# Kernel tuning notes

Measured on AMD Instinct MI355X. Metric: run time of the kernel, lower is better.

## Reference

```python
import jax, jax.numpy as jnp
import numpy as np

B, T, F, H = 128, 512, 256, 512


def setup_inputs() -> dict:
    key = jax.random.key(0)
    k1, k2, k3, k4 = jax.random.split(key, 4)
    scale_k = 1.0 / np.sqrt(F)
    scale_r = 1.0 / np.sqrt(H)
    return {
        "x": jax.random.normal(k1, (B, T, F), dtype=jnp.float32),
        "kernel": jax.random.normal(k2, (F, 4 * H), dtype=jnp.float32) * scale_k,
        "recurrent_kernel": jax.random.normal(k3, (H, 4 * H), dtype=jnp.float32) * scale_r,
        "bias": jax.random.normal(k4, (4 * H,), dtype=jnp.float32) * 0.01,
    }


def _lstm(x, kernel, recurrent_kernel, bias):
    # x: [B, T, F] -> scan over time. Keras gate order: i, f, g(cell), o.
    h0 = jnp.zeros((x.shape[0], H), dtype=x.dtype)
    c0 = jnp.zeros((x.shape[0], H), dtype=x.dtype)
    # Precompute input projections for all timesteps in one big GEMM: [B,T,4H]
    xz = jnp.einsum('btf,fg->btg', x, kernel) + bias

    def step(carry, xz_t):
        h, c = carry
        z = xz_t + h @ recurrent_kernel  # [B, 4H]
        i, f, g, o = jnp.split(z, 4, axis=-1)
        i = jax.nn.sigmoid(i)
        f = jax.nn.sigmoid(f)
        g = jnp.tanh(g)
        o = jax.nn.sigmoid(o)
        c_new = f * c + i * g
        h_new = o * jnp.tanh(c_new)
        return (h_new, c_new), h_new

    (h_last, c_last), hs = jax.lax.scan(step, (h0, c0), jnp.swapaxes(xz, 0, 1))
    output = jnp.swapaxes(hs, 0, 1)  # [B, T, H]
    return output, h_last, c_last


def reference(x, kernel, recurrent_kernel, bias):
    # Inference-mode forward (dropout inactive), matching Keras LSTM eval behavior.
    output, h, c = _lstm(x, kernel, recurrent_kernel, bias)
    return (output, h, c)
```

## Files before the change

### kernel.cpp

```cpp
#include <hip/hip_runtime.h>
#include <stdint.h>


#define Bb 128
#define Tt 512
#define Ff 256
#define Hh 512
#define G4 2048
#define SENT 0xFFFFFFFFu

typedef __attribute__((ext_vector_type(8))) short short8;
typedef __attribute__((ext_vector_type(4))) float floatx4;
typedef __attribute__((ext_vector_type(4))) unsigned int uint4v;

__device__ __forceinline__ unsigned short f2bf(float f) {
    unsigned u = __float_as_uint(f);
    return (unsigned short)((u + 0x7FFFu + ((u >> 16) & 1u)) >> 16);
}
__device__ __forceinline__ float bf2f(unsigned short h) {
    return __uint_as_float(((unsigned)h) << 16);
}
__device__ __forceinline__ float sigm(float x) { return 1.f / (1.f + __expf(-x)); }
__device__ __forceinline__ float tanh_f(float x) {
    float e = __expf(-2.f * fabsf(x));
    return copysignf((1.f - e) / (1.f + e), x);
}

__global__ __launch_bounds__(256, 2) void lstm_xz(
    const float* __restrict__ x, const float* __restrict__ w,
    const float* __restrict__ bias, _Float16* __restrict__ xzh)
{
    __shared__ unsigned short Ahi[128 * 40];
    __shared__ unsigned short Alo[128 * 40];
    __shared__ unsigned short Wt [128 * 40];

    const int tid = threadIdx.x;
    int idx = blockIdx.x;
    int xcd = idx & 7;
    int chunk = idx >> 3;
    int msup = chunk >> 7;
    int s = chunk & 127;
    int nt = s >> 3;
    int mi0 = s & 7;
    int mt = xcd * 64 + msup * 8 + mi0;
    const int m0 = mt << 7;
    const int n0 = nt << 7;

    const int lane = tid & 63;
    const int wv = tid >> 6;
    const int wm = wv >> 1, wn = wv & 1;
    const int cB = lane & 15, kgrp = lane >> 4;

    floatx4 acc[4][4];
#pragma unroll
    for (int i = 0; i < 4; ++i)
#pragma unroll
        for (int j = 0; j < 4; ++j) acc[i][j] = (floatx4){0.f, 0.f, 0.f, 0.f};

    float bv[4];
#pragma unroll
    for (int ni = 0; ni < 4; ++ni) bv[ni] = bias[n0 + wn * 64 + ni * 16 + cB];

    for (int it = 0; it < 8; ++it) {
        const int k0 = it * 32;
#pragma unroll
        for (int sw = 0; sw < 4; ++sw) {
            int e = sw * 256 + tid;
            int row = e >> 3, kq = e & 7;
            float4 v = *((const float4*)(x + (size_t)(m0 + row) * Ff + k0) + kq);
            unsigned short h0 = f2bf(v.x), h1 = f2bf(v.y), h2 = f2bf(v.z), h3 = f2bf(v.w);
            unsigned short l0 = f2bf(v.x - bf2f(h0)), l1 = f2bf(v.y - bf2f(h1));
            unsigned short l2 = f2bf(v.z - bf2f(h2)), l3 = f2bf(v.w - bf2f(h3));
            uint2 ph, pl;
            ph.x = (unsigned)h0 | ((unsigned)h1 << 16); ph.y = (unsigned)h2 | ((unsigned)h3 << 16);
            pl.x = (unsigned)l0 | ((unsigned)l1 << 16); pl.y = (unsigned)l2 | ((unsigned)l3 << 16);
            *(uint2*)(&Ahi[row * 40 + kq * 4]) = ph;
            *(uint2*)(&Alo[row * 40 + kq * 4]) = pl;
        }
#pragma unroll
        for (int sw = 0; sw < 4; ++sw) {
            int e = sw * 256 + tid;
            int kr = e >> 5, nq = e & 31;
            float4 v = *((const float4*)(w + (size_t)(k0 + kr) * G4 + n0) + nq);
            int nb = nq * 4;
            Wt[(nb + 0) * 40 + kr] = f2bf(v.x);
            Wt[(nb + 1) * 40 + kr] = f2bf(v.y);
            Wt[(nb + 2) * 40 + kr] = f2bf(v.z);
            Wt[(nb + 3) * 40 + kr] = f2bf(v.w);
        }
        __syncthreads();

        short8 bfr[4];
#pragma unroll
        for (int ni = 0; ni < 4; ++ni)
            bfr[ni] = *(const short8*)(&Wt[(wn * 64 + ni * 16 + cB) * 40 + kgrp * 8]);
#pragma unroll
        for (int mi = 0; mi < 4; ++mi) {
            short8 ah = *(const short8*)(&Ahi[(wm * 64 + mi * 16 + cB) * 40 + kgrp * 8]);
            short8 al = *(const short8*)(&Alo[(wm * 64 + mi * 16 + cB) * 40 + kgrp * 8]);
#pragma unroll
            for (int ni = 0; ni < 4; ++ni) {
                acc[mi][ni] = __builtin_amdgcn_mfma_f32_16x16x32_bf16(ah, bfr[ni], acc[mi][ni], 0, 0, 0);
                acc[mi][ni] = __builtin_amdgcn_mfma_f32_16x16x32_bf16(al, bfr[ni], acc[mi][ni], 0, 0, 0);
            }
        }
        __syncthreads();
    }
#pragma unroll
    for (int mi = 0; mi < 4; ++mi)
#pragma unroll
        for (int ni = 0; ni < 4; ++ni) {
            int rowb = m0 + wm * 64 + mi * 16 + kgrp * 4;
            int col = n0 + wn * 64 + ni * 16 + cB;
#pragma unroll
            for (int rr = 0; rr < 4; ++rr)
                xzh[(size_t)(rowb + rr) * G4 + col] = (_Float16)(acc[mi][ni][rr] + bv[ni]);
        }
}

__global__ __launch_bounds__(256, 1) void lstm_rec(
    const _Float16* __restrict__ xzh, const float* __restrict__ rk,
    unsigned* __restrict__ hbuf_u, float* __restrict__ out)
{
    __shared__ unsigned short Rlds[128 * 512];

    const int tid = threadIdx.x;
    const int idx = blockIdx.x;
    const int rg = idx & 7;
    const int cb = idx >> 3;
    const int b0 = rg * 16;
    const int hc0 = cb * 32;

    const int lane = tid & 63;
    const int wv = tid >> 6;
    const int cB = lane & 15, kgrp = lane >> 4;
    const int hcw = hc0 + wv * 8;
    const int c7 = cB & 7;
    const int col = hcw + c7;
    const bool hi = (cB & 8) != 0;

    for (int e = tid; e < 64 * 512; e += 256) {
        int p = e & 63, k = e >> 6;
        int n0 = 2 * p;
        int loc = n0 & 31, w = n0 >> 5;
        int gate = ((loc >> 4) << 1) | ((loc >> 3) & 1);
        int gcol = gate * Hh + hc0 + w * 8 + (loc & 7);
        float2 v = *(const float2*)(rk + (size_t)k * G4 + gcol);
        Rlds[n0 * 512 + (k ^ ((n0 & 7) << 3))] = f2bf(v.x);
        Rlds[(n0 + 1) * 512 + (k ^ (((n0 + 1) & 7) << 3))] = f2bf(v.y);
    }

    const unsigned* xz_u = (const unsigned*)xzh;
    const unsigned* pr[4];
#pragma unroll
    for (int r = 0; r < 4; ++r)
        pr[r] = xz_u + ((size_t)(b0 + kgrp * 4 + r) * Tt * G4 + (col & ~1)) / 2;

    float xzr[16];
#pragma unroll
    for (int g = 0; g < 4; ++g)
#pragma unroll
        for (int r = 0; r < 4; ++r) {
            unsigned v = pr[r][g * 256];
            xzr[g * 4 + r] = (float)__builtin_bit_cast(_Float16,
                (unsigned short)((col & 1) ? (v >> 16) : (v & 0xffffu)));
        }
#pragma unroll
    for (int r = 0; r < 4; ++r) pr[r] += G4 / 2;

    __syncthreads();

    short8 bf0[16], bf1[16];
    {
        const int nb = wv * 32;
        const int swz = c7 << 3;
#pragma unroll
        for (int kk = 0; kk < 16; ++kk) {
            int kb = (kk * 32 + kgrp * 8) ^ swz;
            bf0[kk] = *(const short8*)&Rlds[(nb + cB) * 512 + kb];
            bf1[kk] = *(const short8*)&Rlds[(nb + 16 + cB) * 512 + kb];
        }
    }
    __syncthreads();

    float creg[4] = {0.f, 0.f, 0.f, 0.f};
    unsigned* const gbase = hbuf_u + (size_t)rg * 4 * 4096;

    for (int t = 0; t < Tt; ++t) {
        const bool last = (t == Tt - 1);

        unsigned pf[16];
        if (!last) {
#pragma unroll
            for (int g = 0; g < 4; ++g)
#pragma unroll
                for (int r = 0; r < 4; ++r)
                    pf[g * 4 + r] = pr[r][g * 256];
        }

        floatx4 acc0 = (floatx4){0.f, 0.f, 0.f, 0.f};
        floatx4 acc1 = (floatx4){0.f, 0.f, 0.f, 0.f};

        if (t > 0) {
            unsigned short* const hs = (t & 1) ? (Rlds + 16 * 512) : Rlds;
            unsigned* const hcu = (unsigned*)hs;

            {
                const unsigned* sb = gbase + ((t - 1) & 3) * 4096;
                const unsigned* q0 = sb + (wv + 0) * 256 + 4 * lane;
                const unsigned* q1 = sb + (wv + 4) * 256 + 4 * lane;
                const unsigned* q2 = sb + (wv + 8) * 256 + 4 * lane;
                const unsigned* q3 = sb + (wv + 12) * 256 + 4 * lane;
                uint4v v0, v1, v2, v3;
                asm volatile("global_load_dwordx4 %0, %1, off sc0 sc1" : "=v"(v0) : "v"(q0) : "memory");
                asm volatile("global_load_dwordx4 %0, %1, off sc0 sc1" : "=v"(v1) : "v"(q1) : "memory");
                asm volatile("global_load_dwordx4 %0, %1, off sc0 sc1" : "=v"(v2) : "v"(q2) : "memory");
                asm volatile("global_load_dwordx4 %0, %1, off sc0 sc1" : "=v"(v3) : "v"(q3) : "memory");
                asm volatile("s_waitcnt vmcnt(0)" ::: "memory");
                while (__any((v0[0] == SENT) | (v0[1] == SENT) | (v0[2] == SENT) | (v0[3] == SENT))) {
                    asm volatile("global_load_dwordx4 %0, %1, off sc0 sc1" : "=v"(v0) : "v"(q0) : "memory");
                    asm volatile("s_waitcnt vmcnt(0)" ::: "memory");
                }
                *(uint4v*)(hcu + (wv + 0) * 256 + 4 * (lane ^ ((wv + 0) & 7))) = v0;
                while (__any((v1[0] == SENT) | (v1[1] == SENT) | (v1[2] == SENT) | (v1[3] == SENT))) {
                    asm volatile("global_load_dwordx4 %0, %1, off sc0 sc1" : "=v"(v1) : "v"(q1) : "memory");
                    asm volatile("s_waitcnt vmcnt(0)" ::: "memory");
                }
                *(uint4v*)(hcu + (wv + 4) * 256 + 4 * (lane ^ ((wv + 4) & 7))) = v1;
                while (__any((v2[0] == SENT) | (v2[1] == SENT) | (v2[2] == SENT) | (v2[3] == SENT))) {
                    asm volatile("global_load_dwordx4 %0, %1, off sc0 sc1" : "=v"(v2) : "v"(q2) : "memory");
                    asm volatile("s_waitcnt vmcnt(0)" ::: "memory");
                }
                *(uint4v*)(hcu + (wv + 8) * 256 + 4 * (lane ^ ((wv + 8) & 7))) = v2;
                while (__any((v3[0] == SENT) | (v3[1] == SENT) | (v3[2] == SENT) | (v3[3] == SENT))) {
                    asm volatile("global_load_dwordx4 %0, %1, off sc0 sc1" : "=v"(v3) : "v"(q3) : "memory");
                    asm volatile("s_waitcnt vmcnt(0)" ::: "memory");
                }
                *(uint4v*)(hcu + (wv + 12) * 256 + 4 * (lane ^ ((wv + 12) & 7))) = v3;
            }

            if (t >= 2) {
                unsigned* rs = gbase + ((t - 2) & 3) * 4096
                             + (tid >> 4) * 256 + (hc0 >> 1) + (tid & 15);
                __hip_atomic_store(rs, SENT, __ATOMIC_RELAXED, __HIP_MEMORY_SCOPE_AGENT);
            }

            __syncthreads();

            floatx4 e0 = (floatx4){0.f, 0.f, 0.f, 0.f};
            floatx4 e1 = (floatx4){0.f, 0.f, 0.f, 0.f};
            const int swz = c7 << 3;
#pragma unroll
            for (int kk = 0; kk < 16; kk += 2) {
                int kb0 = (kk * 32 + kgrp * 8) ^ swz;
                int kb1 = ((kk + 1) * 32 + kgrp * 8) ^ swz;
                short8 a0 = *(const short8*)&hs[cB * 512 + kb0];
                short8 a1 = *(const short8*)&hs[cB * 512 + kb1];
                acc0 = __builtin_amdgcn_mfma_f32_16x16x32_bf16(a0, bf0[kk], acc0, 0, 0, 0);
                acc1 = __builtin_amdgcn_mfma_f32_16x16x32_bf16(a0, bf1[kk], acc1, 0, 0, 0);
                e0 = __builtin_amdgcn_mfma_f32_16x16x32_bf16(a1, bf0[kk + 1], e0, 0, 0, 0);
                e1 = __builtin_amdgcn_mfma_f32_16x16x32_bf16(a1, bf1[kk + 1], e1, 0, 0, 0);
            }
            acc0 = acc0 + e0;
            acc1 = acc1 + e1;
        }

        float hv[4];
#pragma unroll
        for (int r = 0; r < 4; ++r) {
            float a0 = acc0[r], a1 = acc1[r];
            float a0x = __shfl_xor(a0, 8);
            float a1x = __shfl_xor(a1, 8);
            float zi = (hi ? a0x : a0) + xzr[0 * 4 + r];
            float zf = (hi ? a0 : a0x) + xzr[1 * 4 + r];
            float zg = (hi ? a1x : a1) + xzr[2 * 4 + r];
            float zo = (hi ? a1 : a1x) + xzr[3 * 4 + r];
            creg[r] = sigm(zf) * creg[r] + sigm(zi) * tanh_f(zg);
            hv[r] = sigm(zo) * tanh_f(creg[r]);
        }

        float hn[4];
#pragma unroll
        for (int r = 0; r < 4; ++r) hn[r] = __shfl_xor(hv[r], 1);
        const bool ew = (!hi && !(cB & 1));

        if (!last) {
            unsigned* wbase = gbase + (t & 3) * 4096;
#pragma unroll
            for (int r = 0; r < 4; ++r) {
                if (ew) {
                    unsigned hp = (unsigned)f2bf(hv[r]) | ((unsigned)f2bf(hn[r]) << 16);
                    __hip_atomic_store(wbase + (kgrp * 4 + r) * 256 + (col >> 1), hp,
                                       __ATOMIC_RELAXED, __HIP_MEMORY_SCOPE_AGENT);
                }
            }
        }

#pragma unroll
        for (int r = 0; r < 4; ++r) {
            if (ew) {
                size_t b = (size_t)(b0 + kgrp * 4 + r);
                *(float2*)(out + (b * Tt + (size_t)t) * Hh + col) = make_float2(hv[r], hn[r]);
            }
        }

        if (last) {
            float* hl = out + (size_t)Bb * Tt * Hh;
            float* cl = hl + (size_t)Bb * Hh;
#pragma unroll
            for (int r = 0; r < 4; ++r) {
                float cn = __shfl_xor(creg[r], 1);
                if (ew) {
                    size_t b = (size_t)(b0 + kgrp * 4 + r);
                    *(float2*)(hl + b * Hh + col) = make_float2(hv[r], hn[r]);
                    *(float2*)(cl + b * Hh + col) = make_float2(creg[r], cn);
                }
            }
            break;
        }

#pragma unroll
        for (int i = 0; i < 16; ++i)
            xzr[i] = (float)__builtin_bit_cast(_Float16,
                (unsigned short)((col & 1) ? (pf[i] >> 16) : (pf[i] & 0xffffu)));
#pragma unroll
        for (int r = 0; r < 4; ++r) pr[r] += G4 / 2;
    }
}

extern "C" void kernel_launch(void* const* d_in, const int* in_sizes, int n_in,
                              void* d_out, int out_size, void* d_ws, size_t ws_size,
                              hipStream_t stream) {
    (void)in_sizes; (void)n_in; (void)out_size; (void)ws_size;
    const float* x    = (const float*)d_in[0];
    const float* w    = (const float*)d_in[1];
    const float* rk   = (const float*)d_in[2];
    const float* bias = (const float*)d_in[3];
    float* out = (float*)d_out;

    char* ws = (char*)d_ws;
    const size_t XZ_BYTES   = (size_t)Bb * Tt * G4 * sizeof(_Float16);
    const size_t HBUF_BYTES = (size_t)8 * 4 * 16 * 256 * 4;

    _Float16* xzh = (_Float16*)ws;
    unsigned* hbuf = (unsigned*)(ws + XZ_BYTES);

    hipMemsetAsync(ws + XZ_BYTES, 0xFF, HBUF_BYTES, stream);

    lstm_xz<<<dim3(8192), dim3(256), 0, stream>>>(x, w, bias, xzh);
    lstm_rec<<<dim3(128), dim3(256), 0, stream>>>(xzh, rk, hbuf, out);
}
```

Baseline: 2.236 ms.

## Fuse input projection GEMM into recurrent kernel, computing x·W per timestep

Removes the separate xz GEMM kernel and its fp16 intermediate buffer. Each recurrent block now keeps its slice of the input kernel in registers, stages x[t+1] as hi/lo bf16 in LDS (double-buffered), and runs the extra MFMAs each step alongside the hidden-state exchange. This eliminates the large xz write and read and one launch. The cost is extra MFMA work and x loads on the serial critical path of every timestep, using only 128 blocks.

```diff
diff --git a/kernel.cpp b/kernel.cpp
--- a/kernel.cpp
+++ b/kernel.cpp
@@ -8,6 +8,7 @@
 #define Hh 512
 #define G4 2048
 #define SENT 0xFFFFFFFFu
+#define XB 16384
 
 typedef __attribute__((ext_vector_type(8))) short short8;
 typedef __attribute__((ext_vector_type(4))) float floatx4;
@@ -26,100 +27,33 @@
     return copysignf((1.f - e) / (1.f + e), x);
 }
 
-__global__ __launch_bounds__(256, 2) void lstm_xz(
-    const float* __restrict__ x, const float* __restrict__ w,
-    const float* __restrict__ bias, _Float16* __restrict__ xzh)
-{
-    __shared__ unsigned short Ahi[128 * 40];
-    __shared__ unsigned short Alo[128 * 40];
-    __shared__ unsigned short Wt [128 * 40];
-
-    const int tid = threadIdx.x;
-    int idx = blockIdx.x;
-    int xcd = idx & 7;
-    int chunk = idx >> 3;
-    int msup = chunk >> 7;
-    int s = chunk & 127;
-    int nt = s >> 3;
-    int mi0 = s & 7;
-    int mt = xcd * 64 + msup * 8 + mi0;
-    const int m0 = mt << 7;
-    const int n0 = nt << 7;
-
-    const int lane = tid & 63;
-    const int wv = tid >> 6;
-    const int wm = wv >> 1, wn = wv & 1;
-    const int cB = lane & 15, kgrp = lane >> 4;
-
-    floatx4 acc[4][4];
-#pragma unroll
-    for (int i = 0; i < 4; ++i)
-#pragma unroll
-        for (int j = 0; j < 4; ++j) acc[i][j] = (floatx4){0.f, 0.f, 0.f, 0.f};
-
-    float bv[4];
-#pragma unroll
-    for (int ni = 0; ni < 4; ++ni) bv[ni] = bias[n0 + wn * 64 + ni * 16 + cB];
-
-    for (int it = 0; it < 8; ++it) {
-        const int k0 = it * 32;
-#pragma unroll
-        for (int sw = 0; sw < 4; ++sw) {
-            int e = sw * 256 + tid;
-            int row = e >> 3, kq = e & 7;
-            float4 v = *((const float4*)(x + (size_t)(m0 + row) * Ff + k0) + kq);
-            unsigned short h0 = f2bf(v.x), h1 = f2bf(v.y), h2 = f2bf(v.z), h3 = f2bf(v.w);
-            unsigned short l0 = f2bf(v.x - bf2f(h0)), l1 = f2bf(v.y - bf2f(h1));
-            unsigned short l2 = f2bf(v.z - bf2f(h2)), l3 = f2bf(v.w - bf2f(h3));
-            uint2 ph, pl;
-            ph.x = (unsigned)h0 | ((unsigned)h1 << 16); ph.y = (unsigned)h2 | ((unsigned)h3 << 16);
-            pl.x = (unsigned)l0 | ((unsigned)l1 << 16); pl.y = (unsigned)l2 | ((unsigned)l3 << 16);
-            *(uint2*)(&Ahi[row * 40 + kq * 4]) = ph;
-            *(uint2*)(&Alo[row * 40 + kq * 4]) = pl;
-        }
-#pragma unroll
-        for (int sw = 0; sw < 4; ++sw) {
-            int e = sw * 256 + tid;
-            int kr = e >> 5, nq = e & 31;
-            float4 v = *((const float4*)(w + (size_t)(k0 + kr) * G4 + n0) + nq);
-            int nb = nq * 4;
-            Wt[(nb + 0) * 40 + kr] = f2bf(v.x);
-            Wt[(nb + 1) * 40 + kr] = f2bf(v.y);
-            Wt[(nb + 2) * 40 + kr] = f2bf(v.z);
-            Wt[(nb + 3) * 40 + kr] = f2bf(v.w);
-        }
-        __syncthreads();
-
-        short8 bfr[4];
-#pragma unroll
-        for (int ni = 0; ni < 4; ++ni)
-            bfr[ni] = *(const short8*)(&Wt[(wn * 64 + ni * 16 + cB) * 40 + kgrp * 8]);
-#pragma unroll
-        for (int mi = 0; mi < 4; ++mi) {
-            short8 ah = *(const short8*)(&Ahi[(wm * 64 + mi * 16 + cB) * 40 + kgrp * 8]);
-            short8 al = *(const short8*)(&Alo[(wm * 64 + mi * 16 + cB) * 40 + kgrp * 8]);
-#pragma unroll
-            for (int ni = 0; ni < 4; ++ni) {
-                acc[mi][ni] = __builtin_amdgcn_mfma_f32_16x16x32_bf16(ah, bfr[ni], acc[mi][ni], 0, 0, 0);
-                acc[mi][ni] = __builtin_amdgcn_mfma_f32_16x16x32_bf16(al, bfr[ni], acc[mi][ni], 0, 0, 0);
-            }
-        }
-        __syncthreads();
-    }
-#pragma unroll
-    for (int mi = 0; mi < 4; ++mi)
-#pragma unroll
-        for (int ni = 0; ni < 4; ++ni) {
-            int rowb = m0 + wm * 64 + mi * 16 + kgrp * 4;
-            int col = n0 + wn * 64 + ni * 16 + cB;
-#pragma unroll
-            for (int rr = 0; rr < 4; ++rr)
-                xzh[(size_t)(rowb + rr) * G4 + col] = (_Float16)(acc[mi][ni][rr] + bv[ni]);
-        }
+__device__ __forceinline__ void xconv_write(const float* xf, unsigned short* xd,
+                                            int row, int kq) {
+    unsigned short hs_[16], ls_[16];
+#pragma unroll
+    for (int j = 0; j < 16; ++j) {
+        hs_[j] = f2bf(xf[j]);
+        ls_[j] = f2bf(xf[j] - bf2f(hs_[j]));
+    }
+    uint4v h0, h1, l0, l1;
+#pragma unroll
+    for (int j = 0; j < 4; ++j) {
+        h0[j] = (unsigned)hs_[2 * j]     | ((unsigned)hs_[2 * j + 1] << 16);
+        h1[j] = (unsigned)hs_[8 + 2 * j] | ((unsigned)hs_[8 + 2 * j + 1] << 16);
+        l0[j] = (unsigned)ls_[2 * j]     | ((unsigned)ls_[2 * j + 1] << 16);
+        l1[j] = (unsigned)ls_[8 + 2 * j] | ((unsigned)ls_[8 + 2 * j + 1] << 16);
+    }
+    const int c0 = (kq * 2) ^ (row & 7);
+    const int c1 = (kq * 2 + 1) ^ (row & 7);
+    *(uint4v*)&xd[row * 256 + c0 * 8] = h0;
+    *(uint4v*)&xd[row * 256 + c1 * 8] = h1;
+    *(uint4v*)&xd[4096 + row * 256 + c0 * 8] = l0;
+    *(uint4v*)&xd[4096 + row * 256 + c1 * 8] = l1;
 }
 
 __global__ __launch_bounds__(256, 1) void lstm_rec(
-    const _Float16* __restrict__ xzh, const float* __restrict__ rk,
+    const float* __restrict__ x, const float* __restrict__ kern,
+    const float* __restrict__ rk, const float* __restrict__ bias,
     unsigned* __restrict__ hbuf_u, float* __restrict__ out)
 {
     __shared__ unsigned short Rlds[128 * 512];
@@ -134,10 +68,10 @@
     const int lane = tid & 63;
     const int wv = tid >> 6;
     const int cB = lane & 15, kgrp = lane >> 4;
-    const int hcw = hc0 + wv * 8;
     const int c7 = cB & 7;
-    const int col = hcw + c7;
+    const int col = hc0 + wv * 8 + c7;
     const bool hi = (cB & 8) != 0;
+    const int xrow = tid >> 4, xkq = tid & 15;
 
     for (int e = tid; e < 64 * 512; e += 256) {
         int p = e & 63, k = e >> 6;
@@ -149,27 +83,7 @@
         Rlds[n0 * 512 + (k ^ ((n0 & 7) << 3))] = f2bf(v.x);
         Rlds[(n0 + 1) * 512 + (k ^ (((n0 + 1) & 7) << 3))] = f2bf(v.y);
     }
-
-    const unsigned* xz_u = (const unsigned*)xzh;
-    const unsigned* pr[4];
-#pragma unroll
-    for (int r = 0; r < 4; ++r)
-        pr[r] = xz_u + ((size_t)(b0 + kgrp * 4 + r) * Tt * G4 + (col & ~1)) / 2;
-
-    float xzr[16];
-#pragma unroll
-    for (int g = 0; g < 4; ++g)
-#pragma unroll
-        for (int r = 0; r < 4; ++r) {
-            unsigned v = pr[r][g * 256];
-            xzr[g * 4 + r] = (float)__builtin_bit_cast(_Float16,
-                (unsigned short)((col & 1) ? (v >> 16) : (v & 0xffffu)));
-        }
-#pragma unroll
-    for (int r = 0; r < 4; ++r) pr[r] += G4 / 2;
-
-    __syncthreads();
-
+    __syncthreads();
     short8 bf0[16], bf1[16];
     {
         const int nb = wv * 32;
@@ -183,79 +97,131 @@
     }
     __syncthreads();
 
+    for (int e = tid; e < 64 * 256; e += 256) {
+        int p = e & 63, k = e >> 6;
+        int n0 = 2 * p;
+        int loc = n0 & 31, w = n0 >> 5;
+        int gate = ((loc >> 4) << 1) | ((loc >> 3) & 1);
+        int gcol = gate * Hh + hc0 + w * 8 + (loc & 7);
+        float2 v = *(const float2*)(kern + (size_t)k * G4 + gcol);
+        Rlds[n0 * 256 + (k ^ ((n0 & 7) << 3))] = f2bf(v.x);
+        Rlds[(n0 + 1) * 256 + (k ^ (((n0 + 1) & 7) << 3))] = f2bf(v.y);
+    }
+    __syncthreads();
+    short8 wf0[8], wf1[8];
+    {
+        const int nb = wv * 32;
+        const int swz = c7 << 3;
+#pragma unroll
+        for (int kk = 0; kk < 8; ++kk) {
+            int kb = (kk * 32 + kgrp * 8) ^ swz;
+            wf0[kk] = *(const short8*)&Rlds[(nb + cB) * 256 + kb];
+            wf1[kk] = *(const short8*)&Rlds[(nb + 16 + cB) * 256 + kb];
+        }
+    }
+    const float bi = bias[0 * Hh + col], bff = bias[1 * Hh + col];
+    const float bg = bias[2 * Hh + col], bo = bias[3 * Hh + col];
+    __syncthreads();
+
+    {
+        float xf[16];
+        const float* xp = x + ((size_t)(b0 + xrow) * Tt + 0) * Ff + xkq * 16;
+#pragma unroll
+        for (int j = 0; j < 4; ++j) *(float4*)(&xf[4 * j]) = ((const float4*)xp)[j];
+        xconv_write(xf, Rlds + XB, xrow, xkq);
+    }
+    __syncthreads();
+
     float creg[4] = {0.f, 0.f, 0.f, 0.f};
     unsigned* const gbase = hbuf_u + (size_t)rg * 4 * 4096;
+    const bool ew = (!hi && !(cB & 1));
+    const int swz = c7 << 3;
 
     for (int t = 0; t < Tt; ++t) {
         const bool last = (t == Tt - 1);
 
-        unsigned pf[16];
+        float xf[16];
         if (!last) {
-#pragma unroll
-            for (int g = 0; g < 4; ++g)
-#pragma unroll
-                for (int r = 0; r < 4; ++r)
-                    pf[g * 4 + r] = pr[r][g * 256];
+            const float* xp = x + ((size_t)(b0 + xrow) * Tt + (t + 1)) * Ff + xkq * 16;
+#pragma unroll
+            for (int j = 0; j < 4; ++j) *(float4*)(&xf[4 * j]) = ((const float4*)xp)[j];
+        }
+
+        floatx4 xza0 = (floatx4){0.f, 0.f, 0.f, 0.f};
+        floatx4 xza1 = (floatx4){0.f, 0.f, 0.f, 0.f};
+        {
+            const unsigned short* xb = Rlds + XB + (t & 1) * 8192;
+#pragma unroll
+            for (int kk = 0; kk < 8; ++kk) {
+                int kb = (kk * 32 + kgrp * 8) ^ swz;
+                short8 ah = *(const short8*)&xb[cB * 256 + kb];
+                short8 al = *(const short8*)&xb[4096 + cB * 256 + kb];
+                xza0 = __builtin_amdgcn_mfma_f32_16x16x32_bf16(ah, wf0[kk], xza0, 0, 0, 0);
+                xza0 = __builtin_amdgcn_mfma_f32_16x16x32_bf16(al, wf0[kk], xza0, 0, 0, 0);
+                xza1 = __builtin_amdgcn_mfma_f32_16x16x32_bf16(ah, wf1[kk], xza1, 0, 0, 0);
+                xza1 = __builtin_amdgcn_mfma_f32_16x16x32_bf16(al, wf1[kk], xza1, 0, 0, 0);
+            }
         }
 
         floatx4 acc0 = (floatx4){0.f, 0.f, 0.f, 0.f};
         floatx4 acc1 = (floatx4){0.f, 0.f, 0.f, 0.f};
+        unsigned short* const hst = Rlds + ((t & 1) ? 8192 : 0);
+        unsigned* const hcu = (unsigned*)hst;
 
         if (t > 0) {
-            unsigned short* const hs = (t & 1) ? (Rlds + 16 * 512) : Rlds;
-            unsigned* const hcu = (unsigned*)hs;
-
-            {
-                const unsigned* sb = gbase + ((t - 1) & 3) * 4096;
-                const unsigned* q0 = sb + (wv + 0) * 256 + 4 * lane;
-                const unsigned* q1 = sb + (wv + 4) * 256 + 4 * lane;
-                const unsigned* q2 = sb + (wv + 8) * 256 + 4 * lane;
-                const unsigned* q3 = sb + (wv + 12) * 256 + 4 * lane;
-                uint4v v0, v1, v2, v3;
+            const unsigned* sb = gbase + ((t - 1) & 3) * 4096;
+            const unsigned* q0 = sb + (wv + 0) * 256 + 4 * lane;
+            const unsigned* q1 = sb + (wv + 4) * 256 + 4 * lane;
+            const unsigned* q2 = sb + (wv + 8) * 256 + 4 * lane;
+            const unsigned* q3 = sb + (wv + 12) * 256 + 4 * lane;
+            uint4v v0, v1, v2, v3;
+            asm volatile("global_load_dwordx4 %0, %1, off sc0 sc1" : "=v"(v0) : "v"(q0) : "memory");
+            asm volatile("global_load_dwordx4 %0, %1, off sc0 sc1" : "=v"(v1) : "v"(q1) : "memory");
+            asm volatile("global_load_dwordx4 %0, %1, off sc0 sc1" : "=v"(v2) : "v"(q2) : "memory");
+            asm volatile("global_load_dwordx4 %0, %1, off sc0 sc1" : "=v"(v3) : "v"(q3) : "memory");
+            asm volatile("s_waitcnt vmcnt(0)" ::: "memory");
+            while (__any((v0[0] == SENT) | (v0[1] == SENT) | (v0[2] == SENT) | (v0[3] == SENT))) {
                 asm volatile("global_load_dwordx4 %0, %1, off sc0 sc1" : "=v"(v0) : "v"(q0) : "memory");
+                asm volatile("s_waitcnt vmcnt(0)" ::: "memory");
+            }
+            *(uint4v*)(hcu + (wv + 0) * 256 + 4 * (lane ^ ((wv + 0) & 7))) = v0;
+            while (__any((v1[0] == SENT) | (v1[1] == SENT) | (v1[2] == SENT) | (v1[3] == SENT))) {
                 asm volatile("global_load_dwordx4 %0, %1, off sc0 sc1" : "=v"(v1) : "v"(q1) : "memory");
+                asm volatile("s_waitcnt vmcnt(0)" ::: "memory");
+            }
+            *(uint4v*)(hcu + (wv + 4) * 256 + 4 * (lane ^ ((wv + 4) & 7))) = v1;
+            while (__any((v2[0] == SENT) | (v2[1] == SENT) | (v2[2] == SENT) | (v2[3] == SENT))) {
                 asm volatile("global_load_dwordx4 %0, %1, off sc0 sc1" : "=v"(v2) : "v"(q2) : "memory");
+                asm volatile("s_waitcnt vmcnt(0)" ::: "memory");
+            }
+            *(uint4v*)(hcu + (wv + 8) * 256 + 4 * (lane ^ ((wv + 8) & 7))) = v2;
+            while (__any((v3[0] == SENT) | (v3[1] == SENT) | (v3[2] == SENT) | (v3[3] == SENT))) {
                 asm volatile("global_load_dwordx4 %0, %1, off sc0 sc1" : "=v"(v3) : "v"(q3) : "memory");
                 asm volatile("s_waitcnt vmcnt(0)" ::: "memory");
-                while (__any((v0[0] == SENT) | (v0[1] == SENT) | (v0[2] == SENT) | (v0[3] == SENT))) {
-                    asm volatile("global_load_dwordx4 %0, %1, off sc0 sc1" : "=v"(v0) : "v"(q0) : "memory");
-                    asm volatile("s_waitcnt vmcnt(0)" ::: "memory");
-                }
-                *(uint4v*)(hcu + (wv + 0) * 256 + 4 * (lane ^ ((wv + 0) & 7))) = v0;
-                while (__any((v1[0] == SENT) | (v1[1] == SENT) | (v1[2] == SENT) | (v1[3] == SENT))) {
-                    asm volatile("global_load_dwordx4 %0, %1, off sc0 sc1" : "=v"(v1) : "v"(q1) : "memory");
-                    asm volatile("s_waitcnt vmcnt(0)" ::: "memory");
-                }
-                *(uint4v*)(hcu + (wv + 4) * 256 + 4 * (lane ^ ((wv + 4) & 7))) = v1;
-                while (__any((v2[0] == SENT) | (v2[1] == SENT) | (v2[2] == SENT) | (v2[3] == SENT))) {
-                    asm volatile("global_load_dwordx4 %0, %1, off sc0 sc1" : "=v"(v2) : "v"(q2) : "memory");
-                    asm volatile("s_waitcnt vmcnt(0)" ::: "memory");
-                }
-                *(uint4v*)(hcu + (wv + 8) * 256 + 4 * (lane ^ ((wv + 8) & 7))) = v2;
-                while (__any((v3[0] == SENT) | (v3[1] == SENT) | (v3[2] == SENT) | (v3[3] == SENT))) {
-                    asm volatile("global_load_dwordx4 %0, %1, off sc0 sc1" : "=v"(v3) : "v"(q3) : "memory");
-                    asm volatile("s_waitcnt vmcnt(0)" ::: "memory");
-                }
-                *(uint4v*)(hcu + (wv + 12) * 256 + 4 * (lane ^ ((wv + 12) & 7))) = v3;
-            }
+            }
+            *(uint4v*)(hcu + (wv + 12) * 256 + 4 * (lane ^ ((wv + 12) & 7))) = v3;
 
             if (t >= 2) {
                 unsigned* rs = gbase + ((t - 2) & 3) * 4096
                              + (tid >> 4) * 256 + (hc0 >> 1) + (tid & 15);
                 __hip_atomic_store(rs, SENT, __ATOMIC_RELAXED, __HIP_MEMORY_SCOPE_AGENT);
             }
-
-            __syncthreads();
-
+        }
+
+        if (!last)
+            xconv_write(xf, Rlds + XB + ((t + 1) & 1) * 8192, xrow, xkq);
+
+        __syncthreads();
+
+        if (t > 0) {
             floatx4 e0 = (floatx4){0.f, 0.f, 0.f, 0.f};
             floatx4 e1 = (floatx4){0.f, 0.f, 0.f, 0.f};
-            const int swz = c7 << 3;
 #pragma unroll
             for (int kk = 0; kk < 16; kk += 2) {
                 int kb0 = (kk * 32 + kgrp * 8) ^ swz;
                 int kb1 = ((kk + 1) * 32 + kgrp * 8) ^ swz;
-                short8 a0 = *(const short8*)&hs[cB * 512 + kb0];
-                short8 a1 = *(const short8*)&hs[cB * 512 + kb1];
+                short8 a0 = *(const short8*)&hst[cB * 512 + kb0];
+                short8 a1 = *(const short8*)&hst[cB * 512 + kb1];
                 acc0 = __builtin_amdgcn_mfma_f32_16x16x32_bf16(a0, bf0[kk], acc0, 0, 0, 0);
                 acc1 = __builtin_amdgcn_mfma_f32_16x16x32_bf16(a0, bf1[kk], acc1, 0, 0, 0);
                 e0 = __builtin_amdgcn_mfma_f32_16x16x32_bf16(a1, bf0[kk + 1], e0, 0, 0, 0);
@@ -265,16 +231,18 @@
             acc1 = acc1 + e1;
         }
 
+        floatx4 s0 = acc0 + xza0;
+        floatx4 s1 = acc1 + xza1;
         float hv[4];
 #pragma unroll
         for (int r = 0; r < 4; ++r) {
-            float a0 = acc0[r], a1 = acc1[r];
-            float a0x = __shfl_xor(a0, 8);
-            float a1x = __shfl_xor(a1, 8);
-            float zi = (hi ? a0x : a0) + xzr[0 * 4 + r];
-            float zf = (hi ? a0 : a0x) + xzr[1 * 4 + r];
-            float zg = (hi ? a1x : a1) + xzr[2 * 4 + r];
-            float zo = (hi ? a1 : a1x) + xzr[3 * 4 + r];
+            float f0 = s0[r], f1 = s1[r];
+            float f0x = __shfl_xor(f0, 8);
+            float f1x = __shfl_xor(f1, 8);
+            float zi = (hi ? f0x : f0) + bi;
+            float zf = (hi ? f0 : f0x) + bff;
+            float zg = (hi ? f1x : f1) + bg;
+            float zo = (hi ? f1 : f1x) + bo;
             creg[r] = sigm(zf) * creg[r] + sigm(zi) * tanh_f(zg);
             hv[r] = sigm(zo) * tanh_f(creg[r]);
         }
@@ -282,7 +250,6 @@
         float hn[4];
 #pragma unroll
         for (int r = 0; r < 4; ++r) hn[r] = __shfl_xor(hv[r], 1);
-        const bool ew = (!hi && !(cB & 1));
 
         if (!last) {
             unsigned* wbase = gbase + (t & 3) * 4096;
@@ -294,17 +261,14 @@
                                        __ATOMIC_RELAXED, __HIP_MEMORY_SCOPE_AGENT);
                 }
             }
-        }
-
-#pragma unroll
-        for (int r = 0; r < 4; ++r) {
-            if (ew) {
-                size_t b = (size_t)(b0 + kgrp * 4 + r);
-                *(float2*)(out + (b * Tt + (size_t)t) * Hh + col) = make_float2(hv[r], hn[r]);
-            }
-        }
-
-        if (last) {
+#pragma unroll
+            for (int r = 0; r < 4; ++r) {
+                if (ew) {
+                    size_t b = (size_t)(b0 + kgrp * 4 + r);
+                    *(float2*)(out + (b * Tt + (size_t)t) * Hh + col) = make_float2(hv[r], hn[r]);
+                }
+            }
+        } else {
             float* hl = out + (size_t)Bb * Tt * Hh;
             float* cl = hl + (size_t)Bb * Hh;
 #pragma unroll
@@ -312,19 +276,13 @@
                 float cn = __shfl_xor(creg[r], 1);
                 if (ew) {
                     size_t b = (size_t)(b0 + kgrp * 4 + r);
+                    *(float2*)(out + (b * Tt + (size_t)t) * Hh + col) = make_float2(hv[r], hn[r]);
                     *(float2*)(hl + b * Hh + col) = make_float2(hv[r], hn[r]);
                     *(float2*)(cl + b * Hh + col) = make_float2(creg[r], cn);
                 }
             }
             break;
         }
-
-#pragma unroll
-        for (int i = 0; i < 16; ++i)
-            xzr[i] = (float)__builtin_bit_cast(_Float16,
-                (unsigned short)((col & 1) ? (pf[i] >> 16) : (pf[i] & 0xffffu)));
-#pragma unroll
-        for (int r = 0; r < 4; ++r) pr[r] += G4 / 2;
     }
 }
 
@@ -338,15 +296,10 @@
     const float* bias = (const float*)d_in[3];
     float* out = (float*)d_out;
 
-    char* ws = (char*)d_ws;
-    const size_t XZ_BYTES   = (size_t)Bb * Tt * G4 * sizeof(_Float16);
     const size_t HBUF_BYTES = (size_t)8 * 4 * 16 * 256 * 4;
-
-    _Float16* xzh = (_Float16*)ws;
-    unsigned* hbuf = (unsigned*)(ws + XZ_BYTES);
-
-    hipMemsetAsync(ws + XZ_BYTES, 0xFF, HBUF_BYTES, stream);
-
-    lstm_xz<<<dim3(8192), dim3(256), 0, stream>>>(x, w, bias, xzh);
-    lstm_rec<<<dim3(128), dim3(256), 0, stream>>>(xzh, rk, hbuf, out);
-}
+    unsigned* hbuf = (unsigned*)d_ws;
+
+    hipMemsetAsync(d_ws, 0xFF, HBUF_BYTES, stream);
+
+    lstm_rec<<<dim3(128), dim3(256), 0, stream>>>(x, w, rk, bias, hbuf, out);
+}
```

Measured after the change: 2.069 ms. 7.5% less time.
